# Optimization experiments

Hardware: AMD Instinct MI355X
Metric: run time of the kernel (lower is better)

Reference implementation:

```python
import jax, jax.numpy as jnp
import numpy as np

_P = ((0, 0), (1, 1), (1, 1), (0, 0))  # pad 1 on H and W (mypadding with sigma_fill=0)

_SHAPES = [
    ("e1a", (3, 3, 3, 64)), ("e1b", (3, 3, 64, 64)),
    ("e2a", (3, 3, 64, 128)), ("e2b", (3, 3, 128, 128)),
    ("ba", (3, 3, 128, 256)), ("bb", (3, 3, 256, 256)),
    ("d2u", (3, 3, 256, 128)), ("d2a", (3, 3, 256, 128)), ("d2b", (3, 3, 128, 128)),
    ("d1u", (3, 3, 128, 64)), ("d1a", (3, 3, 128, 64)), ("d1b", (3, 3, 64, 64)),
    ("fin", (1, 1, 64, 2)),
]


def _conv(x, w):
    return jax.lax.conv_general_dilated(x, w, (1, 1), 'VALID',
                                        dimension_numbers=('NHWC', 'HWIO', 'NHWC'))


def _conv_input(x, w_mu, w_sig):
    # mu = conv(x, w_mu); sigma = (sum over patch of x^2) * softplus(w_sigma)
    mu = _conv(x, w_mu)
    ws = jax.nn.softplus(w_sig)
    k, _, cin, _ = w_mu.shape
    ones = jnp.ones((k, k, cin, 1), x.dtype)
    s = _conv(x * x, ones) * ws
    return mu, s


def _conv_inter(x, s_in, w_mu, w_sig):
    # sigma = x^2 (x) w_sig + s_in (x) w_mu^2 + s_in (x) w_sig   (patch-sum form)
    mu = _conv(x, w_mu)
    ws = jax.nn.softplus(w_sig)
    k, _, cin, _ = w_mu.shape
    ones = jnp.ones((k, k, cin, 1), x.dtype)
    s = (_conv(x * x, ones) + _conv(s_in, ones)) * ws + _conv(s_in, w_mu * w_mu)
    return mu, s


def _relu(mu, s):
    g = (mu > 0).astype(mu.dtype)  # grad of ReLU; g^2 == g
    return jnp.maximum(mu, 0.0), g * s


def _pool(mu, s):
    # 2x2/stride-2 max pool with argmax; sigma gathered at argmax locations
    B, H, W, C = mu.shape

    def win(t):
        return t.reshape(B, H // 2, 2, W // 2, 2, C).transpose(0, 1, 3, 5, 2, 4).reshape(
            B, H // 2, W // 2, C, 4)

    mw, sw = win(mu), win(s)
    idx = jnp.argmax(mw, axis=-1)[..., None]
    mu_out = jnp.take_along_axis(mw, idx, axis=-1)[..., 0]
    s_out = jnp.take_along_axis(sw, idx, axis=-1)[..., 0]
    return mu_out, s_out


def _unpool(x):
    # zero-insertion: out[b, 2i+1, 2j+1, c] = x[b, i, j, c]; shape [B, 2H+1, 2W+1, C]
    B, H, W, C = x.shape
    out = jnp.zeros((B, 2 * H + 1, 2 * W + 1, C), x.dtype)
    return out.at[:, 1::2, 1::2, :].set(x)


def _crop(enc, dec):
    dh = (enc.shape[1] - dec.shape[1]) // 2
    dw = (enc.shape[2] - dec.shape[2]) // 2
    return enc[:, dh:dh + dec.shape[1], dw:dw + dec.shape[2], :]


def _softmax_prop(mu, s):
    B, H, W, C = mu.shape
    m = mu.reshape(B, -1, C)
    sg = s.reshape(B, -1, C)
    p = jax.nn.softmax(m, axis=-1)
    eye = jnp.eye(C, dtype=p.dtype)
    grad = p[..., :, None] * eye - p[..., :, None] * p[..., None, :]  # diag(p) - p p^T
    s_out = jnp.einsum('bnij,bnj->bni', grad * grad, sg)
    return p, s_out


def setup_inputs() -> dict:
    key = jax.random.key(0)
    out = {"x": jax.random.normal(jax.random.fold_in(key, 999), (4, 128, 128, 3), dtype=jnp.float32)}
    for i, (name, sh) in enumerate(_SHAPES):
        out[f"w_mu_{name}"] = 0.1 * jax.random.normal(jax.random.fold_in(key, i), sh, dtype=jnp.float32)
        out[f"w_sig_{name}"] = jax.random.uniform(jax.random.fold_in(key, 100 + i), (sh[-1],),
                                                  minval=-12.0, maxval=-4.6, dtype=jnp.float32)
    return out


def reference(x, w_mu_e1a, w_sig_e1a, w_mu_e1b, w_sig_e1b, w_mu_e2a, w_sig_e2a,
              w_mu_e2b, w_sig_e2b, w_mu_ba, w_sig_ba, w_mu_bb, w_sig_bb,
              w_mu_d2u, w_sig_d2u, w_mu_d2a, w_sig_d2a, w_mu_d2b, w_sig_d2b,
              w_mu_d1u, w_sig_d1u, w_mu_d1a, w_sig_d1a, w_mu_d1b, w_sig_d1b,
              w_mu_fin, w_sig_fin):
    # encoder level 1
    mu, s = _conv_input(jnp.pad(x, _P), w_mu_e1a, w_sig_e1a)
    mu, s = _relu(mu, s)
    mu, s = _conv_inter(jnp.pad(mu, _P), jnp.pad(s, _P), w_mu_e1b, w_sig_e1b)
    muE1, sE1 = _relu(mu, s)                       # [4,128,128,64]
    mu, s = _pool(muE1, sE1)                       # [4,64,64,64]
    # encoder level 2
    mu, s = _conv_inter(jnp.pad(mu, _P), jnp.pad(s, _P), w_mu_e2a, w_sig_e2a)
    mu, s = _relu(mu, s)
    mu, s = _conv_inter(jnp.pad(mu, _P), jnp.pad(s, _P), w_mu_e2b, w_sig_e2b)
    muE2, sE2 = _relu(mu, s)                       # [4,64,64,128]
    mu, s = _pool(muE2, sE2)                       # [4,32,32,128]
    # bottleneck
    mu, s = _conv_inter(jnp.pad(mu, _P), jnp.pad(s, _P), w_mu_ba, w_sig_ba)
    mu, s = _relu(mu, s)
    mu, s = _conv_inter(jnp.pad(mu, _P), jnp.pad(s, _P), w_mu_bb, w_sig_bb)
    mu, s = _relu(mu, s)                           # [4,32,32,256]
    # decoder level 2
    mu, s = _unpool(mu), _unpool(s)                # [4,65,65,256]
    mu, s = _conv_inter(mu, s, w_mu_d2u, w_sig_d2u)  # VALID -> [4,63,63,128]
    mu, s = _relu(mu, s)
    mu = jnp.concatenate([mu, _crop(muE2, mu)], axis=-1)
    s = jnp.concatenate([s, _crop(sE2, s)], axis=-1)  # [4,63,63,256]
    mu, s = _conv_inter(jnp.pad(mu, _P), jnp.pad(s, _P), w_mu_d2a, w_sig_d2a)
    mu, s = _relu(mu, s)
    mu, s = _conv_inter(jnp.pad(mu, _P), jnp.pad(s, _P), w_mu_d2b, w_sig_d2b)
    mu, s = _relu(mu, s)                           # [4,63,63,128]
    # decoder level 1
    mu, s = _unpool(mu), _unpool(s)                # [4,127,127,128]
    mu, s = _conv_inter(mu, s, w_mu_d1u, w_sig_d1u)  # VALID -> [4,125,125,64]
    mu, s = _relu(mu, s)
    mu = jnp.concatenate([mu, _crop(muE1, mu)], axis=-1)
    s = jnp.concatenate([s, _crop(sE1, s)], axis=-1)  # [4,125,125,128]
    mu, s = _conv_inter(jnp.pad(mu, _P), jnp.pad(s, _P), w_mu_d1a, w_sig_d1a)
    mu, s = _relu(mu, s)
    mu, s = _conv_inter(jnp.pad(mu, _P), jnp.pad(s, _P), w_mu_d1b, w_sig_d1b)
    mu, s = _relu(mu, s)
    # 1x1 classification conv + pixel-wise softmax density propagation
    mu, s = _conv_inter(mu, s, w_mu_fin, w_sig_fin)  # [4,125,125,2]
    return _softmax_prop(mu, s)                      # ([4,15625,2], [4,15625,2])
```

## Files before the change

kernel.cpp:

```cpp
#include <hip/hip_runtime.h>
#include <math.h>


typedef __attribute__((ext_vector_type(8))) short short8;
typedef __attribute__((ext_vector_type(4))) float floatx4;

__device__ __forceinline__ float softplus_f(float x) { return log1pf(expf(x)); }

__device__ __forceinline__ unsigned short f2bf(float x) {
    unsigned int u = __float_as_uint(x);
    u = (u + 0x7FFF + ((u >> 16) & 1)) >> 16;
    return (unsigned short)u;
}
__device__ __forceinline__ float bfval(unsigned short h) {
    return __uint_as_float((unsigned int)h << 16);
}
__device__ __forceinline__ float bf2f_lo(unsigned int u) {
    return __uint_as_float(u << 16);
}
__device__ __forceinline__ float bf2f_hi(unsigned int u) {
    return __uint_as_float(u & 0xFFFF0000u);
}

__global__ void wprep3_kernel(const float* __restrict__ w,
                              unsigned short* __restrict__ wTh,
                              unsigned short* __restrict__ wTl,
                              unsigned short* __restrict__ wTsq,
                              int Cin, int Cout, int n)
{
    int idx = blockIdx.x * blockDim.x + threadIdx.x;
    if (idx >= n) return;
    int per = Cin * Cout;
    int tap = idx / per;
    int rem = idx - tap * per;
    int co = rem / Cin;
    int ci = rem - co * Cin;
    float v = w[(size_t)(tap * Cin + ci) * Cout + co];
    unsigned short hh = f2bf(v);
    wTh[idx] = hh;
    wTl[idx] = f2bf(v - bfval(hh));
    wTsq[idx] = f2bf(v * v);
}

__global__ void sp_kernel(const float* __restrict__ wsig,
                          float* __restrict__ sp, int n)
{
    int i = blockIdx.x * blockDim.x + threadIdx.x;
    if (i < n) sp[i] = softplus_f(wsig[i]);
}

__global__ void t_hl_kernel(const unsigned short* __restrict__ m1h,
                            const unsigned short* __restrict__ m1l,
                            const unsigned short* __restrict__ s1h,
                            const unsigned short* __restrict__ s1l,
                            const unsigned short* __restrict__ m2h,
                            const unsigned short* __restrict__ m2l,
                            const unsigned short* __restrict__ s2h,
                            const unsigned short* __restrict__ s2l,
                            float* __restrict__ t_out,
                            int B_, int Hin, int Win, int Cin1, int Cin2,
                            int H2, int W2, int dh, int dw)
{
    int pix = blockIdx.x * blockDim.x + threadIdx.x;
    int total = B_ * Hin * Win;
    if (pix >= total) return;
    float acc = 0.f;
    {
        const unsigned short* mh = m1h + (size_t)pix * Cin1;
        const unsigned short* ml = m1l + (size_t)pix * Cin1;
        const unsigned short* sh = s1h + (size_t)pix * Cin1;
        const unsigned short* sl = s1l + (size_t)pix * Cin1;
        for (int ci = 0; ci < Cin1; ci += 8) {
            uint4 vmh = *(const uint4*)(mh + ci);
            uint4 vml = *(const uint4*)(ml + ci);
            uint4 vsh = *(const uint4*)(sh + ci);
            uint4 vsl = *(const uint4*)(sl + ci);
            float m0 = bf2f_lo(vmh.x) + bf2f_lo(vml.x), m1 = bf2f_hi(vmh.x) + bf2f_hi(vml.x);
            float m2 = bf2f_lo(vmh.y) + bf2f_lo(vml.y), m3 = bf2f_hi(vmh.y) + bf2f_hi(vml.y);
            float m4 = bf2f_lo(vmh.z) + bf2f_lo(vml.z), m5 = bf2f_hi(vmh.z) + bf2f_hi(vml.z);
            float m6 = bf2f_lo(vmh.w) + bf2f_lo(vml.w), m7 = bf2f_hi(vmh.w) + bf2f_hi(vml.w);
            acc += m0*m0 + m1*m1 + m2*m2 + m3*m3 + m4*m4 + m5*m5 + m6*m6 + m7*m7;
            acc += bf2f_lo(vsh.x) + bf2f_hi(vsh.x) + bf2f_lo(vsh.y) + bf2f_hi(vsh.y)
                 + bf2f_lo(vsh.z) + bf2f_hi(vsh.z) + bf2f_lo(vsh.w) + bf2f_hi(vsh.w);
            acc += bf2f_lo(vsl.x) + bf2f_hi(vsl.x) + bf2f_lo(vsl.y) + bf2f_hi(vsl.y)
                 + bf2f_lo(vsl.z) + bf2f_hi(vsl.z) + bf2f_lo(vsl.w) + bf2f_hi(vsl.w);
        }
    }
    if (Cin2 > 0) {
        int b = pix / (Hin * Win);
        int rem = pix - b * (Hin * Win);
        int h = rem / Win, w = rem - (rem / Win) * Win;
        size_t base = ((size_t)(b * H2 + h + dh) * W2 + (w + dw)) * Cin2;
        const unsigned short* mh = m2h + base;
        const unsigned short* ml = m2l + base;
        const unsigned short* sh = s2h + base;
        const unsigned short* sl = s2l + base;
        for (int ci = 0; ci < Cin2; ci += 8) {
            uint4 vmh = *(const uint4*)(mh + ci);
            uint4 vml = *(const uint4*)(ml + ci);
            uint4 vsh = *(const uint4*)(sh + ci);
            uint4 vsl = *(const uint4*)(sl + ci);
            float m0 = bf2f_lo(vmh.x) + bf2f_lo(vml.x), m1 = bf2f_hi(vmh.x) + bf2f_hi(vml.x);
            float m2 = bf2f_lo(vmh.y) + bf2f_lo(vml.y), m3 = bf2f_hi(vmh.y) + bf2f_hi(vml.y);
            float m4 = bf2f_lo(vmh.z) + bf2f_lo(vml.z), m5 = bf2f_hi(vmh.z) + bf2f_hi(vml.z);
            float m6 = bf2f_lo(vmh.w) + bf2f_lo(vml.w), m7 = bf2f_hi(vmh.w) + bf2f_hi(vml.w);
            acc += m0*m0 + m1*m1 + m2*m2 + m3*m3 + m4*m4 + m5*m5 + m6*m6 + m7*m7;
            acc += bf2f_lo(vsh.x) + bf2f_hi(vsh.x) + bf2f_lo(vsh.y) + bf2f_hi(vsh.y)
                 + bf2f_lo(vsh.z) + bf2f_hi(vsh.z) + bf2f_lo(vsh.w) + bf2f_hi(vsh.w);
            acc += bf2f_lo(vsl.x) + bf2f_hi(vsl.x) + bf2f_lo(vsl.y) + bf2f_hi(vsl.y)
                 + bf2f_lo(vsl.z) + bf2f_hi(vsl.z) + bf2f_lo(vsl.w) + bf2f_hi(vsl.w);
        }
    }
    t_out[pix] = acc;
}

__global__ void q9_kernel(const float* __restrict__ t_in,
                          float* __restrict__ q9, int B_, int H, int W)
{
    int pix = blockIdx.x * blockDim.x + threadIdx.x;
    int total = B_ * H * W;
    if (pix >= total) return;
    int b = pix / (H * W);
    int rem = pix - b * (H * W);
    int h = rem / W, w = rem - (rem / W) * W;
    float acc = 0.f;
    for (int kh = 0; kh < 3; kh++) {
        int ih = h + kh - 1;
        if ((unsigned)ih >= (unsigned)H) continue;
        for (int kw = 0; kw < 3; kw++) {
            int iw = w + kw - 1;
            if ((unsigned)iw >= (unsigned)W) continue;
            acc += t_in[(size_t)(b * H + ih) * W + iw];
        }
    }
    q9[pix] = acc;
}

__global__ void q9u_kernel(const float* __restrict__ t_in,
                           float* __restrict__ q9,
                           int B_, int Hout, int Wout, int Hin, int Win)
{
    int pix = blockIdx.x * blockDim.x + threadIdx.x;
    int total = B_ * Hout * Wout;
    if (pix >= total) return;
    int b = pix / (Hout * Wout);
    int rem = pix - b * (Hout * Wout);
    int ho = rem / Wout, wo = rem - (rem / Wout) * Wout;
    float acc = 0.f;
    for (int kh = 0; kh < 3; kh++) {
        int uh = ho + kh;
        if (!(uh & 1)) continue;
        int ih = (uh - 1) >> 1;
        for (int kw = 0; kw < 3; kw++) {
            int uw = wo + kw;
            if (!(uw & 1)) continue;
            int iw = (uw - 1) >> 1;
            acc += t_in[(size_t)(b * Hin + ih) * Win + iw];
        }
    }
    q9[pix] = acc;
}

__global__ void __launch_bounds__(256)
fused_layer_kernel(const unsigned short* __restrict__ m1h, const unsigned short* __restrict__ m1l,
                   const unsigned short* __restrict__ s1h, const unsigned short* __restrict__ s1l,
                   const unsigned short* __restrict__ m2h, const unsigned short* __restrict__ m2l,
                   const unsigned short* __restrict__ s2h, const unsigned short* __restrict__ s2l,
                   const float* __restrict__ q9v,
                   const unsigned short* __restrict__ wTh, const unsigned short* __restrict__ wTl,
                   const unsigned short* __restrict__ wTsq,
                   const float* __restrict__ spv_,
                   float* __restrict__ oMf, float* __restrict__ oSf,
                   unsigned short* __restrict__ oMh, unsigned short* __restrict__ oMl,
                   unsigned short* __restrict__ oSh, unsigned short* __restrict__ oSl,
                   int B_, int H, int W, int Hin, int Win, int unpoolMode,
                   int Cin1, int Cin2,
                   int H2, int W2, int dh, int dw, int Cout)
{
    __shared__ unsigned short ldsB[3 * 2304];
    const int tid = threadIdx.x;
    const int lane = tid & 63;
    const int wave = tid >> 6;
    const int total = B_ * H * W;
    const int Cin = Cin1 + Cin2;
    const int ntiles = Cout >> 6;
    const int nPixBlk = (total + 63) >> 6;
    const int nReal = nPixBlk * ntiles;
    const int chunk = (int)gridDim.x >> 3;
    int gid = ((int)blockIdx.x & 7) * chunk + ((int)blockIdx.x >> 3);
    if (gid >= nReal) return;
    const int coTile = gid % ntiles;
    const int pixBlk = gid / ntiles;
    const int pixBase = pixBlk * 64 + wave * 16;
    const int coBase = coTile * 64;
    const int row = lane & 15;
    const int quad = lane >> 4;

    const unsigned short* wsel0; const unsigned short* wsel1; const unsigned short* wsel2;
    int tofs0, tofs1, tofs2;
    int ldso0, ldso1, ldso2;
    {
        int u = tid * 3;
        int arr = u >> 8, rem = u & 255, co = rem >> 2, part = rem & 3;
        wsel0 = (arr == 0) ? wTh : (arr == 1) ? wTl : wTsq;
        tofs0 = co * Cin + part * 8;
        ldso0 = arr * 2304 + co * 36 + part * 8;
        u++;
        arr = u >> 8; rem = u & 255; co = rem >> 2; part = rem & 3;
        wsel1 = (arr == 0) ? wTh : (arr == 1) ? wTl : wTsq;
        tofs1 = co * Cin + part * 8;
        ldso1 = arr * 2304 + co * 36 + part * 8;
        u++;
        arr = u >> 8; rem = u & 255; co = rem >> 2; part = rem & 3;
        wsel2 = (arr == 0) ? wTh : (arr == 1) ? wTl : wTsq;
        tofs2 = co * Cin + part * 8;
        ldso2 = arr * 2304 + co * 36 + part * 8;
    }

    int P = pixBase + row;
    bool pv = P < total;
    int Pc = pv ? P : 0;
    int pb = Pc / (H * W);
    int r0i = Pc - pb * (H * W);
    int ph = r0i / W;
    int pw = r0i - ph * W;

    floatx4 accM[4], accS[4];
#pragma unroll
    for (int i = 0; i < 4; i++) {
        accM[i] = (floatx4){0.f, 0.f, 0.f, 0.f};
        accS[i] = (floatx4){0.f, 0.f, 0.f, 0.f};
    }
    const short8 zero8 = {0, 0, 0, 0, 0, 0, 0, 0};

    const size_t tapstep = (size_t)Cout * Cin;
    size_t tapbase = (size_t)coBase * Cin;

    uint4 pf0 = *(const uint4*)(wsel0 + tapbase + tofs0);
    uint4 pf1 = *(const uint4*)(wsel1 + tapbase + tofs1);
    uint4 pf2 = *(const uint4*)(wsel2 + tapbase + tofs2);

    for (int tap = 0; tap < 9; tap++, tapbase += tapstep) {
        int kh = tap / 3, kw = tap - kh * 3;
        int ih, iw;
        bool tv;
        if (unpoolMode) {
            int uh = ph + kh, uw = pw + kw;
            tv = pv && (uh & 1) && (uw & 1);
            ih = (uh - 1) >> 1;
            iw = (uw - 1) >> 1;
        } else {
            ih = ph + kh - 1;
            iw = pw + kw - 1;
            tv = pv && ((unsigned)ih < (unsigned)Hin) && ((unsigned)iw < (unsigned)Win);
        }
        if (!tv) { ih = 0; iw = 0; }
        const int nsrc = (Cin2 > 0) ? 2 : 1;
        for (int src = 0; src < nsrc; src++) {
            const int csrc = src ? Cin2 : Cin1;
            const int cofs = src ? Cin1 : 0;
            const unsigned short* aMhp = src ? m2h : m1h;
            const unsigned short* aMlp = src ? m2l : m1l;
            const unsigned short* aShp = src ? s2h : s1h;
            const unsigned short* aSlp = src ? s2l : s1l;
            size_t ab;
            if (src) ab = ((size_t)(pb * H2 + ih + dh) * W2 + (iw + dw)) * (size_t)Cin2 + quad * 8;
            else     ab = ((size_t)(pb * Hin + ih) * Win + iw) * (size_t)Cin1 + quad * 8;
            for (int kb = 0; kb < csrc; kb += 32) {
                __syncthreads();
                *(uint4*)(&ldsB[ldso0]) = pf0;
                *(uint4*)(&ldsB[ldso1]) = pf1;
                *(uint4*)(&ldsB[ldso2]) = pf2;
                __syncthreads();
                short8 aMh = zero8, aMl = zero8, aSh = zero8, aSl = zero8;
                if (tv) {
                    aMh = *(const short8*)(aMhp + ab + kb);
                    aMl = *(const short8*)(aMlp + ab + kb);
                    aSh = *(const short8*)(aShp + ab + kb);
                    aSl = *(const short8*)(aSlp + ab + kb);
                }
                {
                    int ncol = cofs + kb + 32;
                    size_t nbase;
                    bool hn;
                    if (ncol < Cin) { nbase = tapbase + ncol; hn = true; }
                    else            { nbase = tapbase + tapstep; hn = (tap < 8); }
                    if (hn) {
                        pf0 = *(const uint4*)(wsel0 + nbase + tofs0);
                        pf1 = *(const uint4*)(wsel1 + nbase + tofs1);
                        pf2 = *(const uint4*)(wsel2 + nbase + tofs2);
                    }
                }
#pragma unroll
                for (int nt = 0; nt < 4; nt++) {
                    int lo = (nt * 16 + row) * 36 + quad * 8;
                    short8 bh = *(const short8*)(&ldsB[lo]);
                    short8 bl = *(const short8*)(&ldsB[2304 + lo]);
                    short8 bq = *(const short8*)(&ldsB[4608 + lo]);
                    accM[nt] = __builtin_amdgcn_mfma_f32_16x16x32_bf16(aMh, bh, accM[nt], 0, 0, 0);
                    accM[nt] = __builtin_amdgcn_mfma_f32_16x16x32_bf16(aMl, bh, accM[nt], 0, 0, 0);
                    accM[nt] = __builtin_amdgcn_mfma_f32_16x16x32_bf16(aMh, bl, accM[nt], 0, 0, 0);
                    accM[nt] = __builtin_amdgcn_mfma_f32_16x16x32_bf16(aMl, bl, accM[nt], 0, 0, 0);
                    accS[nt] = __builtin_amdgcn_mfma_f32_16x16x32_bf16(aSh, bq, accS[nt], 0, 0, 0);
                    accS[nt] = __builtin_amdgcn_mfma_f32_16x16x32_bf16(aSl, bq, accS[nt], 0, 0, 0);
                }
            }
        }
    }

#pragma unroll
    for (int nt = 0; nt < 4; nt++) {
        int co = coBase + nt * 16 + row;
        float spv = spv_[co];
        floatx4 am = accM[nt];
        floatx4 as = accS[nt];
#pragma unroll
        for (int r = 0; r < 4; r++) {
            int P2 = pixBase + quad * 4 + r;
            if (P2 < total) {
                size_t o = (size_t)P2 * Cout + co;
                float mu = am[r];
                float s = q9v[P2] * spv + as[r];
                if (!(mu > 0.f)) { mu = 0.f; s = 0.f; }
                if (oMf) oMf[o] = mu;
                if (oSf) oSf[o] = s;
                if (oMh) {
                    unsigned short mh = f2bf(mu);
                    oMh[o] = mh;
                    oMl[o] = f2bf(mu - bfval(mh));
                    unsigned short sh = f2bf(s);
                    oSh[o] = sh;
                    oSl[o] = f2bf(s - bfval(sh));
                }
            }
        }
    }
}

__global__ void conv_input_relu_kernel(const float* __restrict__ x,
                                       const float* __restrict__ w_mu,
                                       const float* __restrict__ w_sig,
                                       unsigned short* __restrict__ m_h,
                                       unsigned short* __restrict__ m_l,
                                       unsigned short* __restrict__ s_h,
                                       unsigned short* __restrict__ s_l,
                                       int B_, int H, int W, int Cin, int Cout)
{
    int co = threadIdx.x;
    int pix = blockIdx.x * blockDim.y + threadIdx.y;
    int total = B_ * H * W;
    if (pix >= total) return;
    int b = pix / (H * W);
    int rem = pix % (H * W);
    int h = rem / W, w = rem % W;

    float mu = 0.f, q = 0.f;
    for (int kh = 0; kh < 3; kh++) {
        int ih = h + kh - 1;
        if (ih < 0 || ih >= H) continue;
        for (int kw = 0; kw < 3; kw++) {
            int iw = w + kw - 1;
            if (iw < 0 || iw >= W) continue;
            const float* xp = x + ((size_t)(b * H + ih) * W + iw) * Cin;
            const float* wp = w_mu + (size_t)((kh * 3 + kw) * Cin) * Cout + co;
            for (int ci = 0; ci < Cin; ci++) {
                float xv = xp[ci];
                mu += xv * wp[(size_t)ci * Cout];
                q += xv * xv;
            }
        }
    }
    float s = q * softplus_f(w_sig[co]);
    if (!(mu > 0.f)) { mu = 0.f; s = 0.f; }
    size_t oidx = (size_t)pix * Cout + co;
    unsigned short mh = f2bf(mu);
    m_h[oidx] = mh;
    m_l[oidx] = f2bf(mu - bfval(mh));
    unsigned short sh = f2bf(s);
    s_h[oidx] = sh;
    s_l[oidx] = f2bf(s - bfval(sh));
}

__global__ void pool_kernel(const float* __restrict__ mu_in,
                            const unsigned short* __restrict__ s_h,
                            const unsigned short* __restrict__ s_l,
                            unsigned short* __restrict__ pm_h,
                            unsigned short* __restrict__ pm_l,
                            unsigned short* __restrict__ ps_h,
                            unsigned short* __restrict__ ps_l,
                            int B_, int H, int W, int C)
{
    int Ho = H / 2, Wo = W / 2;
    size_t total = (size_t)B_ * Ho * Wo * C;
    size_t idx = (size_t)blockIdx.x * blockDim.x + threadIdx.x;
    if (idx >= total) return;
    int c = idx % C;
    size_t t = idx / C;
    int w = t % Wo; t /= Wo;
    int h = t % Ho;
    int b = t / Ho;
    size_t i0 = ((size_t)(b * H + 2 * h) * W + 2 * w) * C + c;
    size_t rowStride = (size_t)W * C;
    float m00 = mu_in[i0], m01 = mu_in[i0 + C];
    float m10 = mu_in[i0 + rowStride], m11 = mu_in[i0 + rowStride + C];
    int best = 0; float bm = m00;
    if (m01 > bm) { bm = m01; best = 1; }
    if (m10 > bm) { bm = m10; best = 2; }
    if (m11 > bm) { bm = m11; best = 3; }
    size_t off = (size_t)(best >> 1) * rowStride + (size_t)(best & 1) * C;
    unsigned short mh = f2bf(bm);
    pm_h[idx] = mh;
    pm_l[idx] = f2bf(bm - bfval(mh));
    ps_h[idx] = s_h[i0 + off];
    ps_l[idx] = s_l[i0 + off];
}

__global__ void final_kernel(const float* __restrict__ mu_in,
                             const float* __restrict__ s_in,
                             const float* __restrict__ w_mu,
                             const float* __restrict__ w_sig,
                             float* __restrict__ out,
                             int B_, int H, int W, int Cin)
{
    int pix = blockIdx.x * blockDim.x + threadIdx.x;
    int total = B_ * H * W;
    if (pix >= total) return;
    const float* mp = mu_in + (size_t)pix * Cin;
    const float* sp = s_in + (size_t)pix * Cin;
    float mu0 = 0.f, mu1 = 0.f, s0a = 0.f, s1a = 0.f, q = 0.f;
    for (int ci = 0; ci < Cin; ci += 4) {
        float4 m = *(const float4*)(mp + ci);
        float4 s = *(const float4*)(sp + ci);
        float4 wa = *(const float4*)(w_mu + ci * 2);
        float4 wb = *(const float4*)(w_mu + ci * 2 + 4);
        mu0 += m.x * wa.x + m.y * wa.z + m.z * wb.x + m.w * wb.z;
        mu1 += m.x * wa.y + m.y * wa.w + m.z * wb.y + m.w * wb.w;
        s0a += s.x * (wa.x * wa.x) + s.y * (wa.z * wa.z) + s.z * (wb.x * wb.x) + s.w * (wb.z * wb.z);
        s1a += s.x * (wa.y * wa.y) + s.y * (wa.w * wa.w) + s.z * (wb.y * wb.y) + s.w * (wb.w * wb.w);
        q += m.x * m.x + s.x + m.y * m.y + s.y + m.z * m.z + s.z + m.w * m.w + s.w;
    }
    float s0 = q * softplus_f(w_sig[0]) + s0a;
    float s1 = q * softplus_f(w_sig[1]) + s1a;
    float mx = fmaxf(mu0, mu1);
    float e0 = expf(mu0 - mx), e1 = expf(mu1 - mx);
    float inv = 1.f / (e0 + e1);
    float p0 = e0 * inv, p1 = e1 * inv;
    float g00 = p0 - p0 * p0, g01 = -p0 * p1;
    float g10 = -p1 * p0,     g11 = p1 - p1 * p1;
    float so0 = g00 * g00 * s0 + g01 * g01 * s1;
    float so1 = g10 * g10 * s0 + g11 * g11 * s1;
    out[(size_t)pix * 2]     = p0;
    out[(size_t)pix * 2 + 1] = p1;
    size_t off = (size_t)total * 2;
    out[off + (size_t)pix * 2]     = so0;
    out[off + (size_t)pix * 2 + 1] = so1;
}


extern "C" void kernel_launch(void* const* d_in, const int* in_sizes, int n_in,
                              void* d_out, int out_size, void* d_ws, size_t ws_size,
                              hipStream_t stream)
{
    const float* x = (const float*)d_in[0];
    enum { E1A, E1B, E2A, E2B, BA, BB, D2U, D2A, D2B, D1U, D1A, D1B, FIN, NW };
    const float* wmu[NW];
    const float* wsig[NW];
    for (int i = 0; i < NW; i++) {
        wmu[i]  = (const float*)d_in[1 + 2 * i];
        wsig[i] = (const float*)d_in[2 + 2 * i];
    }

    const int B_ = 4;
    float* ws = (float*)d_ws;
    float* M0  = ws;
    float* SF  = ws + 4194304;
    float* tq  = ws + 8388608;
    float* q9  = ws + 8454144;
    float* spb = ws + 8519680;
    unsigned short* us = (unsigned short*)(ws + 8521728);
    const size_t NB = 4194304;
    unsigned short* aMh = us;
    unsigned short* aMl = us + NB;
    unsigned short* aSh = us + 2 * NB;
    unsigned short* aSl = us + 3 * NB;
    unsigned short* bMh = us + 4 * NB;
    unsigned short* bMl = us + 5 * NB;
    unsigned short* bSh = us + 6 * NB;
    unsigned short* bSl = us + 7 * NB;
    unsigned short* e1Mh = us + 8 * NB;
    unsigned short* e1Ml = us + 9 * NB;
    unsigned short* e1Sh = us + 10 * NB;
    unsigned short* e1Sl = us + 11 * NB;
    unsigned short* e2Mh = us + 12 * NB;
    unsigned short* e2Ml = e2Mh + 2097152;
    unsigned short* e2Sh = e2Ml + 2097152;
    unsigned short* e2Sl = e2Sh + 2097152;
    unsigned short* wTh  = e2Sl + 2097152;
    unsigned short* wTl  = wTh + 2064384;
    unsigned short* wTsq = wTl + 2064384;

    const int mlay[11]  = {E1B, E2A, E2B, BA, BB, D2U, D2A, D2B, D1U, D1A, D1B};
    const int mcin[11]  = {64, 64, 128, 128, 256, 256, 256, 128, 128, 128, 64};
    const int mcout[11] = {64, 128, 128, 256, 256, 128, 128, 128, 64, 64, 64};
    size_t woff[NW]; int spoff[NW];
    {
        size_t wo = 0; int so = 0;
        for (int i = 0; i < 11; i++) {
            int l = mlay[i];
            woff[l] = wo; spoff[l] = so;
            int n = 9 * mcin[i] * mcout[i];
            wprep3_kernel<<<dim3((n + 255) / 256), dim3(256), 0, stream>>>(
                wmu[l], wTh + wo, wTl + wo, wTsq + wo, mcin[i], mcout[i], n);
            sp_kernel<<<dim3(1), dim3(256), 0, stream>>>(wsig[l], spb + so, mcout[i]);
            wo += n; so += mcout[i];
        }
    }

    auto flayer = [&](const unsigned short* i_mh, const unsigned short* i_ml,
                      const unsigned short* i_sh, const unsigned short* i_sl, int ci1,
                      const unsigned short* k_mh, const unsigned short* k_ml,
                      const unsigned short* k_sh, const unsigned short* k_sl,
                      int ci2, int h2, int w2, int dh, int dw,
                      int H, int W, int widx, int cout,
                      float* oMf, float* oSf,
                      unsigned short* oMh, unsigned short* oMl,
                      unsigned short* oSh, unsigned short* oSl) {
        int total = B_ * H * W;
        t_hl_kernel<<<dim3((total + 255) / 256), dim3(256), 0, stream>>>(
            i_mh, i_ml, i_sh, i_sl, k_mh, k_ml, k_sh, k_sl, tq,
            B_, H, W, ci1, ci2, h2, w2, dh, dw);
        q9_kernel<<<dim3((total + 255) / 256), dim3(256), 0, stream>>>(tq, q9, B_, H, W);
        int nReal = ((total + 63) / 64) * (cout / 64);
        int G = ((nReal + 7) / 8) * 8;
        fused_layer_kernel<<<dim3(G), dim3(256), 0, stream>>>(
            i_mh, i_ml, i_sh, i_sl, k_mh, k_ml, k_sh, k_sl, q9,
            wTh + woff[widx], wTl + woff[widx], wTsq + woff[widx], spb + spoff[widx],
            oMf, oSf, oMh, oMl, oSh, oSl,
            B_, H, W, H, W, 0, ci1, ci2, h2, w2, dh, dw, cout);
    };

    auto ulayer = [&](const unsigned short* i_mh, const unsigned short* i_ml,
                      const unsigned short* i_sh, const unsigned short* i_sl, int ci,
                      int Hin, int Win, int widx, int cout,
                      unsigned short* oMh, unsigned short* oMl,
                      unsigned short* oSh, unsigned short* oSl) {
        int Hout = 2 * Hin - 1, Wout = 2 * Win - 1;
        int nin = B_ * Hin * Win;
        int total = B_ * Hout * Wout;
        t_hl_kernel<<<dim3((nin + 255) / 256), dim3(256), 0, stream>>>(
            i_mh, i_ml, i_sh, i_sl, nullptr, nullptr, nullptr, nullptr, tq,
            B_, Hin, Win, ci, 0, 0, 0, 0, 0);
        q9u_kernel<<<dim3((total + 255) / 256), dim3(256), 0, stream>>>(
            tq, q9, B_, Hout, Wout, Hin, Win);
        int nReal = ((total + 63) / 64) * (cout / 64);
        int G = ((nReal + 7) / 8) * 8;
        fused_layer_kernel<<<dim3(G), dim3(256), 0, stream>>>(
            i_mh, i_ml, i_sh, i_sl, nullptr, nullptr, nullptr, nullptr, q9,
            wTh + woff[widx], wTl + woff[widx], wTsq + woff[widx], spb + spoff[widx],
            nullptr, nullptr, oMh, oMl, oSh, oSl,
            B_, Hout, Wout, Hin, Win, 1, ci, 0, 0, 0, 0, 0, cout);
    };

    {
        int totalPix = B_ * 128 * 128;
        conv_input_relu_kernel<<<dim3((totalPix + 3) / 4), dim3(64, 4), 0, stream>>>(
            x, wmu[E1A], wsig[E1A], aMh, aMl, aSh, aSl, B_, 128, 128, 3, 64);
    }
    flayer(aMh, aMl, aSh, aSl, 64, nullptr, nullptr, nullptr, nullptr, 0, 0, 0, 0, 0,
           128, 128, E1B, 64, M0, nullptr, e1Mh, e1Ml, e1Sh, e1Sl);
    {
        size_t total = (size_t)B_ * 64 * 64 * 64;
        pool_kernel<<<dim3((total + 255) / 256), dim3(256), 0, stream>>>(
            M0, e1Sh, e1Sl, bMh, bMl, bSh, bSl, B_, 128, 128, 64);
    }
    flayer(bMh, bMl, bSh, bSl, 64, nullptr, nullptr, nullptr, nullptr, 0, 0, 0, 0, 0,
           64, 64, E2A, 128, nullptr, nullptr, aMh, aMl, aSh, aSl);
    flayer(aMh, aMl, aSh, aSl, 128, nullptr, nullptr, nullptr, nullptr, 0, 0, 0, 0, 0,
           64, 64, E2B, 128, M0, nullptr, e2Mh, e2Ml, e2Sh, e2Sl);
    {
        size_t total = (size_t)B_ * 32 * 32 * 128;
        pool_kernel<<<dim3((total + 255) / 256), dim3(256), 0, stream>>>(
            M0, e2Sh, e2Sl, bMh, bMl, bSh, bSl, B_, 64, 64, 128);
    }
    flayer(bMh, bMl, bSh, bSl, 128, nullptr, nullptr, nullptr, nullptr, 0, 0, 0, 0, 0,
           32, 32, BA, 256, nullptr, nullptr, aMh, aMl, aSh, aSl);
    flayer(aMh, aMl, aSh, aSl, 256, nullptr, nullptr, nullptr, nullptr, 0, 0, 0, 0, 0,
           32, 32, BB, 256, nullptr, nullptr, bMh, bMl, bSh, bSl);
    ulayer(bMh, bMl, bSh, bSl, 256, 32, 32, D2U, 128, aMh, aMl, aSh, aSl);
    flayer(aMh, aMl, aSh, aSl, 128, e2Mh, e2Ml, e2Sh, e2Sl, 128, 64, 64, 0, 0,
           63, 63, D2A, 128, nullptr, nullptr, bMh, bMl, bSh, bSl);
    flayer(bMh, bMl, bSh, bSl, 128, nullptr, nullptr, nullptr, nullptr, 0, 0, 0, 0, 0,
           63, 63, D2B, 128, nullptr, nullptr, aMh, aMl, aSh, aSl);
    ulayer(aMh, aMl, aSh, aSl, 128, 63, 63, D1U, 64, bMh, bMl, bSh, bSl);
    flayer(bMh, bMl, bSh, bSl, 64, e1Mh, e1Ml, e1Sh, e1Sl, 64, 128, 128, 1, 1,
           125, 125, D1A, 64, nullptr, nullptr, aMh, aMl, aSh, aSl);
    flayer(aMh, aMl, aSh, aSl, 64, nullptr, nullptr, nullptr, nullptr, 0, 0, 0, 0, 0,
           125, 125, D1B, 64, M0, SF, nullptr, nullptr, nullptr, nullptr);
    {
        int totalPix = B_ * 125 * 125;
        final_kernel<<<dim3((totalPix + 63) / 64), dim3(64), 0, stream>>>(
            M0, SF, wmu[FIN], wsig[FIN], (float*)d_out, B_, 125, 125, 64);
    }
}
```

Measured before the change: 1.172 ms.

## Fuse patch sum-of-squares computation into main conv kernel, drop t_hl/q9 passes

Removes the separate per-pixel channel-reduction kernel and the 3x3 neighborhood-sum kernel. The fused conv kernel now accumulates mu^2 + sigma over the A-operand fragments it already loads, reduces across lanes with shuffles, and uses the result in the epilogue. This saves two launches and extra global traffic per layer. In exchange it adds per-element scalar ALU work inside the MFMA inner loop, and relies on the A-fragment load pattern covering every patch element exactly once per output pixel.

```diff
diff --git a/kernel.cpp b/kernel.cpp
--- a/kernel.cpp
+++ b/kernel.cpp
@@ -14,12 +14,6 @@
 }
 __device__ __forceinline__ float bfval(unsigned short h) {
     return __uint_as_float((unsigned int)h << 16);
-}
-__device__ __forceinline__ float bf2f_lo(unsigned int u) {
-    return __uint_as_float(u << 16);
-}
-__device__ __forceinline__ float bf2f_hi(unsigned int u) {
-    return __uint_as_float(u & 0xFFFF0000u);
 }
 
 __global__ void wprep3_kernel(const float* __restrict__ w,
@@ -49,124 +43,11 @@
     if (i < n) sp[i] = softplus_f(wsig[i]);
 }
 
-__global__ void t_hl_kernel(const unsigned short* __restrict__ m1h,
-                            const unsigned short* __restrict__ m1l,
-                            const unsigned short* __restrict__ s1h,
-                            const unsigned short* __restrict__ s1l,
-                            const unsigned short* __restrict__ m2h,
-                            const unsigned short* __restrict__ m2l,
-                            const unsigned short* __restrict__ s2h,
-                            const unsigned short* __restrict__ s2l,
-                            float* __restrict__ t_out,
-                            int B_, int Hin, int Win, int Cin1, int Cin2,
-                            int H2, int W2, int dh, int dw)
-{
-    int pix = blockIdx.x * blockDim.x + threadIdx.x;
-    int total = B_ * Hin * Win;
-    if (pix >= total) return;
-    float acc = 0.f;
-    {
-        const unsigned short* mh = m1h + (size_t)pix * Cin1;
-        const unsigned short* ml = m1l + (size_t)pix * Cin1;
-        const unsigned short* sh = s1h + (size_t)pix * Cin1;
-        const unsigned short* sl = s1l + (size_t)pix * Cin1;
-        for (int ci = 0; ci < Cin1; ci += 8) {
-            uint4 vmh = *(const uint4*)(mh + ci);
-            uint4 vml = *(const uint4*)(ml + ci);
-            uint4 vsh = *(const uint4*)(sh + ci);
-            uint4 vsl = *(const uint4*)(sl + ci);
-            float m0 = bf2f_lo(vmh.x) + bf2f_lo(vml.x), m1 = bf2f_hi(vmh.x) + bf2f_hi(vml.x);
-            float m2 = bf2f_lo(vmh.y) + bf2f_lo(vml.y), m3 = bf2f_hi(vmh.y) + bf2f_hi(vml.y);
-            float m4 = bf2f_lo(vmh.z) + bf2f_lo(vml.z), m5 = bf2f_hi(vmh.z) + bf2f_hi(vml.z);
-            float m6 = bf2f_lo(vmh.w) + bf2f_lo(vml.w), m7 = bf2f_hi(vmh.w) + bf2f_hi(vml.w);
-            acc += m0*m0 + m1*m1 + m2*m2 + m3*m3 + m4*m4 + m5*m5 + m6*m6 + m7*m7;
-            acc += bf2f_lo(vsh.x) + bf2f_hi(vsh.x) + bf2f_lo(vsh.y) + bf2f_hi(vsh.y)
-                 + bf2f_lo(vsh.z) + bf2f_hi(vsh.z) + bf2f_lo(vsh.w) + bf2f_hi(vsh.w);
-            acc += bf2f_lo(vsl.x) + bf2f_hi(vsl.x) + bf2f_lo(vsl.y) + bf2f_hi(vsl.y)
-                 + bf2f_lo(vsl.z) + bf2f_hi(vsl.z) + bf2f_lo(vsl.w) + bf2f_hi(vsl.w);
-        }
-    }
-    if (Cin2 > 0) {
-        int b = pix / (Hin * Win);
-        int rem = pix - b * (Hin * Win);
-        int h = rem / Win, w = rem - (rem / Win) * Win;
-        size_t base = ((size_t)(b * H2 + h + dh) * W2 + (w + dw)) * Cin2;
-        const unsigned short* mh = m2h + base;
-        const unsigned short* ml = m2l + base;
-        const unsigned short* sh = s2h + base;
-        const unsigned short* sl = s2l + base;
-        for (int ci = 0; ci < Cin2; ci += 8) {
-            uint4 vmh = *(const uint4*)(mh + ci);
-            uint4 vml = *(const uint4*)(ml + ci);
-            uint4 vsh = *(const uint4*)(sh + ci);
-            uint4 vsl = *(const uint4*)(sl + ci);
-            float m0 = bf2f_lo(vmh.x) + bf2f_lo(vml.x), m1 = bf2f_hi(vmh.x) + bf2f_hi(vml.x);
-            float m2 = bf2f_lo(vmh.y) + bf2f_lo(vml.y), m3 = bf2f_hi(vmh.y) + bf2f_hi(vml.y);
-            float m4 = bf2f_lo(vmh.z) + bf2f_lo(vml.z), m5 = bf2f_hi(vmh.z) + bf2f_hi(vml.z);
-            float m6 = bf2f_lo(vmh.w) + bf2f_lo(vml.w), m7 = bf2f_hi(vmh.w) + bf2f_hi(vml.w);
-            acc += m0*m0 + m1*m1 + m2*m2 + m3*m3 + m4*m4 + m5*m5 + m6*m6 + m7*m7;
-            acc += bf2f_lo(vsh.x) + bf2f_hi(vsh.x) + bf2f_lo(vsh.y) + bf2f_hi(vsh.y)
-                 + bf2f_lo(vsh.z) + bf2f_hi(vsh.z) + bf2f_lo(vsh.w) + bf2f_hi(vsh.w);
-            acc += bf2f_lo(vsl.x) + bf2f_hi(vsl.x) + bf2f_lo(vsl.y) + bf2f_hi(vsl.y)
-                 + bf2f_lo(vsl.z) + bf2f_hi(vsl.z) + bf2f_lo(vsl.w) + bf2f_hi(vsl.w);
-        }
-    }
-    t_out[pix] = acc;
-}
-
-__global__ void q9_kernel(const float* __restrict__ t_in,
-                          float* __restrict__ q9, int B_, int H, int W)
-{
-    int pix = blockIdx.x * blockDim.x + threadIdx.x;
-    int total = B_ * H * W;
-    if (pix >= total) return;
-    int b = pix / (H * W);
-    int rem = pix - b * (H * W);
-    int h = rem / W, w = rem - (rem / W) * W;
-    float acc = 0.f;
-    for (int kh = 0; kh < 3; kh++) {
-        int ih = h + kh - 1;
-        if ((unsigned)ih >= (unsigned)H) continue;
-        for (int kw = 0; kw < 3; kw++) {
-            int iw = w + kw - 1;
-            if ((unsigned)iw >= (unsigned)W) continue;
-            acc += t_in[(size_t)(b * H + ih) * W + iw];
-        }
-    }
-    q9[pix] = acc;
-}
-
-__global__ void q9u_kernel(const float* __restrict__ t_in,
-                           float* __restrict__ q9,
-                           int B_, int Hout, int Wout, int Hin, int Win)
-{
-    int pix = blockIdx.x * blockDim.x + threadIdx.x;
-    int total = B_ * Hout * Wout;
-    if (pix >= total) return;
-    int b = pix / (Hout * Wout);
-    int rem = pix - b * (Hout * Wout);
-    int ho = rem / Wout, wo = rem - (rem / Wout) * Wout;
-    float acc = 0.f;
-    for (int kh = 0; kh < 3; kh++) {
-        int uh = ho + kh;
-        if (!(uh & 1)) continue;
-        int ih = (uh - 1) >> 1;
-        for (int kw = 0; kw < 3; kw++) {
-            int uw = wo + kw;
-            if (!(uw & 1)) continue;
-            int iw = (uw - 1) >> 1;
-            acc += t_in[(size_t)(b * Hin + ih) * Win + iw];
-        }
-    }
-    q9[pix] = acc;
-}
-
 __global__ void __launch_bounds__(256)
 fused_layer_kernel(const unsigned short* __restrict__ m1h, const unsigned short* __restrict__ m1l,
                    const unsigned short* __restrict__ s1h, const unsigned short* __restrict__ s1l,
                    const unsigned short* __restrict__ m2h, const unsigned short* __restrict__ m2l,
                    const unsigned short* __restrict__ s2h, const unsigned short* __restrict__ s2l,
-                   const float* __restrict__ q9v,
                    const unsigned short* __restrict__ wTh, const unsigned short* __restrict__ wTl,
                    const unsigned short* __restrict__ wTsq,
                    const float* __restrict__ spv_,
@@ -232,6 +113,7 @@
         accS[i] = (floatx4){0.f, 0.f, 0.f, 0.f};
     }
     const short8 zero8 = {0, 0, 0, 0, 0, 0, 0, 0};
+    float qacc = 0.f;
 
     const size_t tapstep = (size_t)Cout * Cin;
     size_t tapbase = (size_t)coBase * Cin;
@@ -278,6 +160,12 @@
                     aMl = *(const short8*)(aMlp + ab + kb);
                     aSh = *(const short8*)(aShp + ab + kb);
                     aSl = *(const short8*)(aSlp + ab + kb);
+#pragma unroll
+                    for (int e = 0; e < 8; e++) {
+                        float m = bfval((unsigned short)aMh[e]) + bfval((unsigned short)aMl[e]);
+                        qacc += m * m
+                              + bfval((unsigned short)aSh[e]) + bfval((unsigned short)aSl[e]);
+                    }
                 }
                 {
                     int ncol = cofs + kb + 32;
@@ -308,6 +196,9 @@
         }
     }
 
+    qacc += __shfl_xor(qacc, 16);
+    qacc += __shfl_xor(qacc, 32);
+
 #pragma unroll
     for (int nt = 0; nt < 4; nt++) {
         int co = coBase + nt * 16 + row;
@@ -317,10 +208,11 @@
 #pragma unroll
         for (int r = 0; r < 4; r++) {
             int P2 = pixBase + quad * 4 + r;
+            float qv = __shfl(qacc, quad * 4 + r);
             if (P2 < total) {
                 size_t o = (size_t)P2 * Cout + co;
                 float mu = am[r];
-                float s = q9v[P2] * spv + as[r];
+                float s = qv * spv + as[r];
                 if (!(mu > 0.f)) { mu = 0.f; s = 0.f; }
                 if (oMf) oMf[o] = mu;
                 if (oSf) oSf[o] = s;
@@ -474,8 +366,6 @@
     float* ws = (float*)d_ws;
     float* M0  = ws;
     float* SF  = ws + 4194304;
-    float* tq  = ws + 8388608;
-    float* q9  = ws + 8454144;
     float* spb = ws + 8519680;
     unsigned short* us = (unsigned short*)(ws + 8521728);
     const size_t NB = 4194304;
@@ -526,14 +416,10 @@
                       unsigned short* oMh, unsigned short* oMl,
                       unsigned short* oSh, unsigned short* oSl) {
         int total = B_ * H * W;
-        t_hl_kernel<<<dim3((total + 255) / 256), dim3(256), 0, stream>>>(
-            i_mh, i_ml, i_sh, i_sl, k_mh, k_ml, k_sh, k_sl, tq,
-            B_, H, W, ci1, ci2, h2, w2, dh, dw);
-        q9_kernel<<<dim3((total + 255) / 256), dim3(256), 0, stream>>>(tq, q9, B_, H, W);
         int nReal = ((total + 63) / 64) * (cout / 64);
         int G = ((nReal + 7) / 8) * 8;
         fused_layer_kernel<<<dim3(G), dim3(256), 0, stream>>>(
-            i_mh, i_ml, i_sh, i_sl, k_mh, k_ml, k_sh, k_sl, q9,
+            i_mh, i_ml, i_sh, i_sl, k_mh, k_ml, k_sh, k_sl,
             wTh + woff[widx], wTl + woff[widx], wTsq + woff[widx], spb + spoff[widx],
             oMf, oSf, oMh, oMl, oSh, oSl,
             B_, H, W, H, W, 0, ci1, ci2, h2, w2, dh, dw, cout);
@@ -545,17 +431,11 @@
                       unsigned short* oMh, unsigned short* oMl,
                       unsigned short* oSh, unsigned short* oSl) {
         int Hout = 2 * Hin - 1, Wout = 2 * Win - 1;
-        int nin = B_ * Hin * Win;
         int total = B_ * Hout * Wout;
-        t_hl_kernel<<<dim3((nin + 255) / 256), dim3(256), 0, stream>>>(
-            i_mh, i_ml, i_sh, i_sl, nullptr, nullptr, nullptr, nullptr, tq,
-            B_, Hin, Win, ci, 0, 0, 0, 0, 0);
-        q9u_kernel<<<dim3((total + 255) / 256), dim3(256), 0, stream>>>(
-            tq, q9, B_, Hout, Wout, Hin, Win);
         int nReal = ((total + 63) / 64) * (cout / 64);
         int G = ((nReal + 7) / 8) * 8;
         fused_layer_kernel<<<dim3(G), dim3(256), 0, stream>>>(
-            i_mh, i_ml, i_sh, i_sl, nullptr, nullptr, nullptr, nullptr, q9,
+            i_mh, i_ml, i_sh, i_sl, nullptr, nullptr, nullptr, nullptr,
             wTh + woff[widx], wTl + woff[widx], wTsq + woff[widx], spb + spoff[widx],
             nullptr, nullptr, oMh, oMl, oSh, oSl,
             B_, Hout, Wout, Hin, Win, 1, ci, 0, 0, 0, 0, 0, cout);
```

After: 1.016 ms. -13.3%, faster.
